# Performance work log

Hardware: AMD Instinct MI355X
Metric: run time of the kernel (lower is better)

Reference implementation:

```python
import jax, jax.numpy as jnp
import numpy as np

B, S, DIM, N, D = 1, 2688, 1536, 12, 128
C = D // 2  # 64 complex pairs per head
EPS = 1e-06


def rms_norm(x, g, eps=EPS):
    # x: [B, S, DIM] -- norm over full model dim, as in WanRMSNorm
    xf = x.astype(jnp.float32)
    return (xf * jax.lax.rsqrt(jnp.mean(xf * xf, axis=-1, keepdims=True) + eps)) * g


def rope_apply(x, f, h, w, freqs_c):
    # x: [B, S, N, D]; freqs_c: complex64 [1024, C]; f*h*w == S (full-seq case)
    s1 = C - 2 * (C // 3)  # 22 (temporal)
    s2 = C // 3            # 21 (height), 21 (width)
    ff = freqs_c[:f, :s1]
    fh = freqs_c[:h, s1:s1 + s2]
    fw = freqs_c[:w, s1 + s2:]
    fi = jnp.concatenate([
        jnp.broadcast_to(ff[:, None, None, :], (f, h, w, s1)),
        jnp.broadcast_to(fh[None, :, None, :], (f, h, w, s2)),
        jnp.broadcast_to(fw[None, None, :, :], (f, h, w, s2)),
    ], axis=-1).reshape(f * h * w, 1, C)  # [S, 1, C]
    xr = x.astype(jnp.float32).reshape(B, S, N, C, 2)
    xc = jax.lax.complex(xr[..., 0], xr[..., 1])          # [B, S, N, C]
    out = xc * fi[None]                                    # broadcast over B, N
    return jnp.stack([out.real, out.imag], axis=-1).reshape(B, S, N, D)


def setup_inputs() -> dict:
    key = jax.random.key(0)
    ks = jax.random.split(key, 12)
    w_scale = 0.02
    # deterministic rope angles (faithful structure: exp(i*theta) per axis slice)
    pos = np.arange(1024, dtype=np.float32)
    inv = 1.0 / (10000.0 ** (np.arange(C, dtype=np.float32) / C))
    ang = pos[:, None] * inv[None, :]
    return {
        "x": jax.random.normal(ks[0], (B, S, DIM), jnp.float32),
        "seq_lens": jnp.full((B,), S, dtype=jnp.int32),
        "grid_sizes": jnp.array([[6, 16, 28]], dtype=jnp.int32),
        "freqs_cos": jnp.asarray(np.cos(ang), jnp.float32),
        "freqs_sin": jnp.asarray(np.sin(ang), jnp.float32),
        "Wq": jax.random.normal(ks[1], (DIM, DIM), jnp.float32) * w_scale,
        "bq": jnp.zeros((DIM,), jnp.float32),
        "Wk": jax.random.normal(ks[2], (DIM, DIM), jnp.float32) * w_scale,
        "bk": jnp.zeros((DIM,), jnp.float32),
        "Wv": jax.random.normal(ks[3], (DIM, DIM), jnp.float32) * w_scale,
        "bv": jnp.zeros((DIM,), jnp.float32),
        "Wo": jax.random.normal(ks[4], (DIM, DIM), jnp.float32) * w_scale,
        "bo": jnp.zeros((DIM,), jnp.float32),
        "gq": jnp.ones((DIM,), jnp.float32),
        "gk": jnp.ones((DIM,), jnp.float32),
    }


def reference(x, seq_lens, grid_sizes, freqs_cos, freqs_sin,
              Wq, bq, Wk, bk, Wv, bv, Wo, bo, gq, gk):
    f, h, w = (int(grid_sizes[0, 0]), int(grid_sizes[0, 1]), int(grid_sizes[0, 2]))
    freqs_c = jax.lax.complex(freqs_cos, freqs_sin)  # [1024, C]

    q = rms_norm(x @ Wq.T + bq, gq).reshape(B, S, N, D)
    k = rms_norm(x @ Wk.T + bk, gk).reshape(B, S, N, D)
    v = (x @ Wv.T + bv).reshape(B, S, N, D)

    q = rope_apply(q, f, h, w, freqs_c)
    k = rope_apply(k, f, h, w, freqs_c)

    # SDPA with key-length masking (k_lens)
    scale = 1.0 / jnp.sqrt(jnp.float32(D))
    scores = jnp.einsum("bqnd,bknd->bnqk", q, k) * scale  # [B, N, S, S]
    kmask = jnp.arange(S)[None, :] < seq_lens[:, None]     # [B, S]
    scores = jnp.where(kmask[:, None, None, :], scores, -jnp.inf)
    attn = jax.nn.softmax(scores, axis=-1)
    out = jnp.einsum("bnqk,bknd->bqnd", attn, v).reshape(B, S, DIM)
    return out @ Wo.T + bo
```

## Files before the change

### kernel.cpp

```cpp
#include <hip/hip_runtime.h>
#include <hip/hip_bf16.h>
#include <stdint.h>

#define S_LEN 2688
#define DIM   1536
#define NH    12
#define HD    128
#define QKV_N 4608

typedef __attribute__((ext_vector_type(8)))  short bf16x8;
typedef __attribute__((ext_vector_type(4)))  float f32x4;
typedef __attribute__((ext_vector_type(16))) float f32x16;

__device__ inline ushort f2bf(float f) {
    uint32_t u = __float_as_uint(f);
    uint32_t r = (u + 0x7fffu + ((u >> 16) & 1u)) >> 16;
    return (ushort)r;
}
__device__ inline float bf2f(uint u) { return __uint_as_float(u << 16); }
__device__ inline float fexp2(float x) {
    float r;
    asm("v_exp_f32 %0, %1" : "=v"(r) : "v"(x));
    return r;
}
__device__ inline uint cvtpk(float lo, float hi) {
    uint r;
    asm("v_cvt_pk_bf16_f32 %0, %1, %2" : "=v"(r) : "v"(lo), "v"(hi));
    return r;
}

#define GLOAD16(gp, lp) __builtin_amdgcn_global_load_lds( \
    (__attribute__((address_space(1))) const void*)(gp),  \
    (__attribute__((address_space(3))) void*)(lp), 16, 0, 0)

__global__ __launch_bounds__(256) void convert_all(
    const float* __restrict__ x,
    const float* __restrict__ wq, const float* __restrict__ wk,
    const float* __restrict__ wv, const float* __restrict__ wo,
    ushort* __restrict__ xb, ushort* __restrict__ wb)
{
    const size_t NX4 = (size_t)S_LEN * DIM / 4;
    const size_t NW4 = (size_t)DIM * DIM / 4;
    size_t i = (size_t)blockIdx.x * 256 + threadIdx.x;
    const float* src; ushort* dst;
    if (i < NX4)            { src = x;  dst = xb; }
    else if (i < NX4+1*NW4) { src = wq; dst = wb;                        i -= NX4; }
    else if (i < NX4+2*NW4) { src = wk; dst = wb + 1*(size_t)DIM*DIM;    i -= NX4+1*NW4; }
    else if (i < NX4+3*NW4) { src = wv; dst = wb + 2*(size_t)DIM*DIM;    i -= NX4+2*NW4; }
    else if (i < NX4+4*NW4) { src = wo; dst = wb + 3*(size_t)DIM*DIM;    i -= NX4+3*NW4; }
    else return;
    float4 v = reinterpret_cast<const float4*>(src)[i];
    ushort4 o = { f2bf(v.x), f2bf(v.y), f2bf(v.z), f2bf(v.w) };
    reinterpret_cast<ushort4*>(dst)[i] = o;
}

__global__ __launch_bounds__(256) void gemm_qkv(
    const ushort* __restrict__ A, const ushort* __restrict__ B,
    const float* __restrict__ bq, const float* __restrict__ bk,
    const float* __restrict__ bv,
    ushort* __restrict__ qkb, ushort* __restrict__ v_t, int K)
{
    __shared__ ushort At[2][128 * 64];
    __shared__ ushort Bt[2][128 * 64];
    const int tid  = threadIdx.x;
    const int wave = tid >> 6, lane = tid & 63;
    const int lid  = blockIdx.y * 21 + blockIdx.x;
    const int xcd  = lid & 7, pos = lid >> 3;
    const int wgid = (xcd < 4 ? xcd * 95 : 4 * 95 + (xcd - 4) * 94) + pos;
    const int m0 = (wgid % 21) * 128, n0 = (wgid / 21) * 128;
    const int wr = wave >> 1, wc = wave & 1;
    const int r = lane & 15, g = lane >> 4;
    const int swz = r & 7;
    const int sj_row[4] = { (0*256+tid)>>3, (1*256+tid)>>3,
                            (2*256+tid)>>3, (3*256+tid)>>3 };
    const int sj_w = tid & 7;

    f32x4 acc[4][4] = {};
    const int NT = K >> 6;

#define STAGE_G(buf, kb)                                                      \
    do {                                                                      \
        const ushort* Ag = A + (size_t)m0 * K + (kb);                         \
        const ushort* Bg = B + (size_t)n0 * K + (kb);                         \
        _Pragma("unroll")                                                     \
        for (int t = 0; t < 4; ++t) {                                         \
            int row = sj_row[t];                                              \
            GLOAD16(Ag + (size_t)row * K + ((sj_w ^ (row & 7)) * 8),          \
                    &At[buf][(t*256 + tid) * 8]);                             \
        }                                                                     \
        _Pragma("unroll")                                                     \
        for (int t = 0; t < 4; ++t) {                                         \
            int row = sj_row[t];                                              \
            GLOAD16(Bg + (size_t)row * K + ((sj_w ^ (row & 7)) * 8),          \
                    &Bt[buf][(t*256 + tid) * 8]);                             \
        }                                                                     \
    } while (0)

    STAGE_G(0, 0);
    asm volatile("s_waitcnt vmcnt(0)" ::: "memory");
    __syncthreads();

    int cur = 0;
    for (int kt = 0; kt < NT; ++kt) {
        if (kt + 1 < NT) STAGE_G(cur ^ 1, (kt+1) * 64);
#pragma unroll
        for (int kk = 0; kk < 2; ++kk) {
            bf16x8 af[4], bfr[4];
#pragma unroll
            for (int i = 0; i < 4; ++i)
                af[i] = *reinterpret_cast<const bf16x8*>(
                    &At[cur][(wr*64 + i*16 + r) * 64 + ((kk*4 + g) ^ swz) * 8]);
#pragma unroll
            for (int i = 0; i < 4; ++i)
                bfr[i] = *reinterpret_cast<const bf16x8*>(
                    &Bt[cur][(wc*64 + i*16 + r) * 64 + ((kk*4 + g) ^ swz) * 8]);
#pragma unroll
            for (int mi = 0; mi < 4; ++mi)
#pragma unroll
                for (int ni = 0; ni < 4; ++ni)
                    acc[mi][ni] = __builtin_amdgcn_mfma_f32_16x16x32_bf16(
                        af[mi], bfr[ni], acc[mi][ni], 0, 0, 0);
        }
        if (kt + 1 < NT) {
            asm volatile("s_waitcnt vmcnt(0)" ::: "memory");
            __syncthreads();
            cur ^= 1;
        }
    }
#undef STAGE_G

    if (n0 < 2*DIM) {
#pragma unroll
        for (int ni = 0; ni < 4; ++ni) {
            int col = n0 + wc*64 + ni*16 + r;
            float bias = (col < DIM) ? bq[col] : bk[col - DIM];
#pragma unroll
            for (int mi = 0; mi < 4; ++mi) {
                int row = m0 + wr*64 + mi*16 + g*4;
#pragma unroll
                for (int j = 0; j < 4; ++j)
                    qkb[(size_t)(row + j) * (2*DIM) + col] =
                        f2bf(acc[mi][ni][j] + bias);
            }
        }
    } else {
#pragma unroll
        for (int ni = 0; ni < 4; ++ni) {
            int d = n0 - 2*DIM + wc*64 + ni*16 + r;
            float bias = bv[d];
#pragma unroll
            for (int mi = 0; mi < 4; ++mi) {
                int row = m0 + wr*64 + mi*16 + g*4;
                uint2 pkt;
                pkt.x = cvtpk(acc[mi][ni][0] + bias, acc[mi][ni][1] + bias);
                pkt.y = cvtpk(acc[mi][ni][2] + bias, acc[mi][ni][3] + bias);
                *reinterpret_cast<uint2*>(&v_t[(size_t)d * S_LEN + row]) = pkt;
            }
        }
    }
}

__global__ __launch_bounds__(256) void gemm_bt2(
    const ushort* __restrict__ A, const ushort* __restrict__ B,
    const float* __restrict__ b0,
    float* __restrict__ C, int M, int N, int K)
{
    __shared__ ushort At[128 * 64];
    __shared__ ushort Bt[64 * 64];
    const int tid  = threadIdx.x;
    const int wave = tid >> 6, lane = tid & 63;
    const int m0 = blockIdx.x * 128, n0 = blockIdx.y * 64;
    const int wr = wave >> 1, wc = wave & 1;
    const int r = lane & 15, g = lane >> 4;
    const int srow = wave * 8 + (lane >> 3);
    const int scol = (lane & 7) * 8;
    const int brow[2] = { (0*256+tid)>>3, (1*256+tid)>>3 };
    const int bcol = (tid & 7) * 8;

    f32x4 acc[4][2] = {};

    for (int k0 = 0; k0 < K; k0 += 64) {
        const ushort* Ag = A + (size_t)m0 * K + k0;
        const ushort* Bg = B + (size_t)n0 * K + k0;
#pragma unroll
        for (int t = 0; t < 4; ++t)
            GLOAD16(Ag + (size_t)(t*32 + srow) * K + scol, &At[t*2048 + wave*512]);
#pragma unroll
        for (int t = 0; t < 2; ++t)
            GLOAD16(Bg + (size_t)brow[t] * K + bcol, &Bt[(t*256 + wave*64) * 8]);
        asm volatile("s_waitcnt vmcnt(0)" ::: "memory");
        __syncthreads();
#pragma unroll
        for (int kk = 0; kk < 2; ++kk) {
            bf16x8 af[4], bfr[2];
#pragma unroll
            for (int i = 0; i < 4; ++i)
                af[i] = *reinterpret_cast<const bf16x8*>(
                    &At[(wr*64 + i*16 + r) * 64 + kk*32 + g*8]);
#pragma unroll
            for (int i = 0; i < 2; ++i)
                bfr[i] = *reinterpret_cast<const bf16x8*>(
                    &Bt[(wc*32 + i*16 + r) * 64 + kk*32 + g*8]);
#pragma unroll
            for (int mi = 0; mi < 4; ++mi)
#pragma unroll
                for (int ni = 0; ni < 2; ++ni)
                    acc[mi][ni] = __builtin_amdgcn_mfma_f32_16x16x32_bf16(
                        af[mi], bfr[ni], acc[mi][ni], 0, 0, 0);
        }
        __syncthreads();
    }

#pragma unroll
    for (int ni = 0; ni < 2; ++ni) {
        int col = n0 + wc*32 + ni*16 + r;
        float bias = b0[col];
#pragma unroll
        for (int mi = 0; mi < 4; ++mi) {
            int row = m0 + wr*64 + mi*16 + g*4;
#pragma unroll
            for (int j = 0; j < 4; ++j)
                C[(size_t)(row + j) * N + col] = acc[mi][ni][j] + bias;
        }
    }
}

__global__ __launch_bounds__(256) void normrope(
    const ushort* __restrict__ qkb, const int* __restrict__ gsz,
    const float* __restrict__ gq, const float* __restrict__ gk,
    const float* __restrict__ fcos, const float* __restrict__ fsin,
    ushort* __restrict__ q_r, ushort* __restrict__ k_r)
{
    const int s   = blockIdx.x;
    const int tid = threadIdx.x;
    const int wave = tid >> 6, lane = tid & 63;
    const uint* qrow = reinterpret_cast<const uint*>(qkb + (size_t)s * (2*DIM));
    const uint* krow = qrow + DIM/2;

    float2 qv[3], kv[3];
    float sq = 0.f, sk = 0.f;
#pragma unroll
    for (int i = 0; i < 3; ++i) {
        int p = tid + i*256;
        uint uq = qrow[p], uk = krow[p];
        qv[i].x = bf2f(uq & 0xffffu); qv[i].y = bf2f(uq >> 16);
        kv[i].x = bf2f(uk & 0xffffu); kv[i].y = bf2f(uk >> 16);
        sq += qv[i].x*qv[i].x + qv[i].y*qv[i].y;
        sk += kv[i].x*kv[i].x + kv[i].y*kv[i].y;
    }
#pragma unroll
    for (int off = 1; off < 64; off <<= 1) {
        sq += __shfl_xor(sq, off);
        sk += __shfl_xor(sk, off);
    }
    __shared__ float red[4][2];
    if (lane == 0) { red[wave][0] = sq; red[wave][1] = sk; }
    __syncthreads();
    sq = red[0][0] + red[1][0] + red[2][0] + red[3][0];
    sk = red[0][1] + red[1][1] + red[2][1] + red[3][1];
    const float rmsq = rsqrtf(sq * (1.f/DIM) + 1e-6f);
    const float rmsk = rsqrtf(sk * (1.f/DIM) + 1e-6f);

    const int hh = gsz[1], ww = gsz[2];
    const int fidx = s / (hh*ww), rem = s % (hh*ww);
    const int hidx = rem / ww,  widx = rem % ww;
    const float qscale = rmsq * (0.08838834764831845f * 1.4426950408889634f);

#pragma unroll
    for (int i = 0; i < 3; ++i) {
        int p = tid + i*256;
        int c = p & 63, head = p >> 6;
        int coord = (c < 22) ? fidx : (c < 43) ? hidx : widx;
        float cv = fcos[coord*64 + c], sv = fsin[coord*64 + c];
        float2 gqv = reinterpret_cast<const float2*>(gq)[p];
        float2 gkv = reinterpret_cast<const float2*>(gk)[p];
        float a = qv[i].x * qscale * gqv.x, b = qv[i].y * qscale * gqv.y;
        uint qo = cvtpk(a*cv - b*sv, a*sv + b*cv);
        a = kv[i].x * rmsk * gkv.x; b = kv[i].y * rmsk * gkv.y;
        uint ko = cvtpk(a*cv - b*sv, a*sv + b*cv);
        size_t off = (((size_t)head * S_LEN + s) * HD + 2*c) >> 1;
        reinterpret_cast<uint*>(q_r)[off] = qo;
        reinterpret_cast<uint*>(k_r)[off] = ko;
    }
}

__global__ __launch_bounds__(256) void attn_fwd(
    const ushort* __restrict__ q_r, const ushort* __restrict__ k_r,
    const ushort* __restrict__ v_t, const int* __restrict__ seq_lens,
    ushort* __restrict__ attn_out)
{
    __shared__ ushort Kl[2][64 * 128];
    __shared__ ushort Vl[2][128 * 64];
    const int tid  = threadIdx.x;
    const int wave = tid >> 6, lane = tid & 63;
    const int n  = blockIdx.y;
    const int seq = seq_lens[0];
    const int khalf = wave & 1, pair = wave >> 1;
    const int ql = lane & 31, h = lane >> 5, sw = lane & 7;
    const int qrow = blockIdx.x * 64 + pair * 32 + ql;
    const ushort* Qh = q_r + (size_t)n * S_LEN * HD;
    const ushort* Kh = k_r + (size_t)n * S_LEN * HD;
    const ushort* Vh = v_t + (size_t)n * HD * S_LEN;

    const int kj_row[4] = { (0*256+tid)>>4, (1*256+tid)>>4, (2*256+tid)>>4, (3*256+tid)>>4 };
    const int kj_w  = tid & 15;
    const int vj_d[4]  = { (0*256+tid)>>3, (1*256+tid)>>3, (2*256+tid)>>3, (3*256+tid)>>3 };
    const int vj_w  = tid & 7;

    bf16x8 qf[8];
#pragma unroll
    for (int c = 0; c < 8; ++c)
        qf[c] = *reinterpret_cast<const bf16x8*>(Qh + (size_t)qrow * HD + c*16 + h*8);

    f32x16 oacc[4] = {};
    float mrun = -1e30f, lrun = 0.f;

    const int nt = (seq + 63) >> 6;

#define STAGE(buf, kbase)                                                     \
    do {                                                                      \
        _Pragma("unroll")                                                     \
        for (int t = 0; t < 4; ++t) {                                         \
            int row = kj_row[t];                                              \
            GLOAD16(Kh + (size_t)((kbase) + row) * HD + ((kj_w ^ (row & 7)) * 8), \
                    &Kl[buf][(t*256 + wave*64) * 8]);                         \
        }                                                                     \
        _Pragma("unroll")                                                     \
        for (int t = 0; t < 4; ++t) {                                         \
            int d = vj_d[t];                                                  \
            GLOAD16(Vh + (size_t)d * S_LEN + (kbase) + ((vj_w ^ (d & 7)) * 8), \
                    &Vl[buf][(t*256 + wave*64) * 8]);                         \
        }                                                                     \
    } while (0)

    STAGE(0, 0);
    asm volatile("s_waitcnt vmcnt(0)" ::: "memory");
    __syncthreads();

    int cur = 0;
    for (int kt = 0; kt < nt; ++kt) {
        const int k0 = kt * 64 + khalf * 32;
        if (kt + 1 < nt) STAGE(cur ^ 1, (kt+1) * 64);

        f32x16 sf = {};
        const ushort* kl = &Kl[cur][(khalf*32 + ql) * 128];
#pragma unroll
        for (int c = 0; c < 8; ++c)
            sf = __builtin_amdgcn_mfma_f32_32x32x16_bf16(
                *reinterpret_cast<const bf16x8*>(kl + ((2*c + h) ^ sw) * 8),
                qf[c], sf, 0, 0, 0);
        if (k0 + 32 > seq) {
#pragma unroll
            for (int j = 0; j < 16; ++j)
                if (k0 + (j&3) + 8*(j>>2) + 4*h >= seq) sf[j] = -1e30f;
        }
        float pm = sf[0];
#pragma unroll
        for (int j = 1; j < 16; ++j) pm = fmaxf(pm, sf[j]);
        pm = fmaxf(pm, __shfl_xor(pm, 32));
        if (!__all(pm - mrun <= 8.f)) {
            float mn = fmaxf(mrun, pm);
            float scl = fexp2(mrun - mn);
            mrun = mn;
            lrun *= scl;
#pragma unroll
            for (int db = 0; db < 4; ++db)
#pragma unroll
                for (int j = 0; j < 16; ++j) oacc[db][j] *= scl;
        }
        float ps = 0.f;
#pragma unroll
        for (int j = 0; j < 16; ++j) {
            float e = fexp2(sf[j] - mrun);
            sf[j] = e;
            ps += e;
        }
        ps += __shfl_xor(ps, 32);
        lrun += ps;
        uint u0 = cvtpk(sf[0],  sf[1]),  u1 = cvtpk(sf[2],  sf[3]);
        uint u2 = cvtpk(sf[4],  sf[5]),  u3 = cvtpk(sf[6],  sf[7]);
        uint u4 = cvtpk(sf[8],  sf[9]),  u5 = cvtpk(sf[10], sf[11]);
        uint u6 = cvtpk(sf[12], sf[13]), u7 = cvtpk(sf[14], sf[15]);
        asm("v_permlane32_swap_b32 %0, %1" : "+v"(u0), "+v"(u2));
        asm("v_permlane32_swap_b32 %0, %1" : "+v"(u1), "+v"(u3));
        asm("v_permlane32_swap_b32 %0, %1" : "+v"(u4), "+v"(u6));
        asm("v_permlane32_swap_b32 %0, %1" : "+v"(u5), "+v"(u7));
        union { uint uu[4]; bf16x8 v; } fa, fb;
        fa.uu[0] = u0; fa.uu[1] = u1; fa.uu[2] = u2; fa.uu[3] = u3;
        fb.uu[0] = u4; fb.uu[1] = u5; fb.uu[2] = u6; fb.uu[3] = u7;
#pragma unroll
        for (int db = 0; db < 4; ++db) {
            const ushort* vl = &Vl[cur][(db*32 + ql) * 64];
            oacc[db] = __builtin_amdgcn_mfma_f32_32x32x16_bf16(
                *reinterpret_cast<const bf16x8*>(vl + ((khalf*4 + 0 + h) ^ sw) * 8),
                fa.v, oacc[db], 0, 0, 0);
            oacc[db] = __builtin_amdgcn_mfma_f32_32x32x16_bf16(
                *reinterpret_cast<const bf16x8*>(vl + ((khalf*4 + 2 + h) ^ sw) * 8),
                fb.v, oacc[db], 0, 0, 0);
        }

        if (kt + 1 < nt) {
            asm volatile("s_waitcnt vmcnt(0)" ::: "memory");
            __syncthreads();
            cur ^= 1;
        }
    }
#undef STAGE

    __syncthreads();
    float* Obuf  = (float*)&Kl[0][0];
    float* MLbuf = (float*)&Vl[0][0];
    if (khalf == 1) {
#pragma unroll
        for (int db = 0; db < 4; ++db)
#pragma unroll
            for (int j = 0; j < 16; ++j) {
                int d = db*32 + (j&3) + 8*(j>>2) + 4*h;
                Obuf[pair*4096 + d*32 + ql] = oacc[db][j];
            }
        if (h == 0) { MLbuf[pair*64 + ql] = mrun; MLbuf[pair*64 + 32 + ql] = lrun; }
    }
    __syncthreads();
    if (khalf == 0) {
        float m2 = MLbuf[pair*64 + ql], l2 = MLbuf[pair*64 + 32 + ql];
        float mm = fmaxf(mrun, m2);
        float s1 = fexp2(mrun - mm), s2 = fexp2(m2 - mm);
        float ltot = lrun * s1 + l2 * s2;
        float inv = (ltot > 0.f) ? 1.f / ltot : 0.f;
#pragma unroll
        for (int db = 0; db < 4; ++db)
#pragma unroll
            for (int j = 0; j < 16; ++j) {
                int d = db*32 + (j&3) + 8*(j>>2) + 4*h;
                oacc[db][j] = (oacc[db][j] * s1 +
                               Obuf[pair*4096 + d*32 + ql] * s2) * inv;
            }
#pragma unroll
        for (int db = 0; db < 4; ++db)
#pragma unroll
            for (int jg = 0; jg < 4; ++jg) {
                uint2 pkt;
                pkt.x = cvtpk(oacc[db][jg*4+0], oacc[db][jg*4+1]);
                pkt.y = cvtpk(oacc[db][jg*4+2], oacc[db][jg*4+3]);
                *reinterpret_cast<uint2*>(
                    &attn_out[(size_t)qrow * DIM + n*HD + db*32 + jg*8 + 4*h]) = pkt;
            }
    }
}

extern "C" void kernel_launch(void* const* d_in, const int* in_sizes, int n_in,
                              void* d_out, int out_size, void* d_ws, size_t ws_size,
                              hipStream_t stream)
{
    const float* x    = (const float*)d_in[0];
    const int*   seqL = (const int*)  d_in[1];
    const int*   gsz  = (const int*)  d_in[2];
    const float* fcos = (const float*)d_in[3];
    const float* fsin = (const float*)d_in[4];
    const float* Wq   = (const float*)d_in[5];
    const float* bq   = (const float*)d_in[6];
    const float* Wk   = (const float*)d_in[7];
    const float* bk   = (const float*)d_in[8];
    const float* Wv   = (const float*)d_in[9];
    const float* bv   = (const float*)d_in[10];
    const float* Wo   = (const float*)d_in[11];
    const float* bo   = (const float*)d_in[12];
    const float* gq   = (const float*)d_in[13];
    const float* gk   = (const float*)d_in[14];
    float* out = (float*)d_out;

    char* ws = (char*)d_ws;
    ushort* xb  = (ushort*)ws;
    ushort* wb  = xb  + (size_t)S_LEN * DIM;
    ushort* qkb = wb  + 4*(size_t)DIM*DIM;
    ushort* v_t = qkb + (size_t)S_LEN * 2*DIM;
    ushort* q_r = v_t + (size_t)DIM * S_LEN;
    ushort* k_r = q_r + (size_t)S_LEN * DIM;
    ushort* ao  = k_r + (size_t)S_LEN * DIM;

    convert_all<<<13248, 256, 0, stream>>>(x, Wq, Wk, Wv, Wo, xb, wb);
    gemm_qkv<<<dim3(21, 36), 256, 0, stream>>>(xb, wb, bq, bk, bv,
                                               qkb, v_t, DIM);
    normrope<<<S_LEN, 256, 0, stream>>>(qkb, gsz, gq, gk, fcos, fsin, q_r, k_r);
    attn_fwd<<<dim3(42, 12), 256, 0, stream>>>(q_r, k_r, v_t, seqL, ao);
    gemm_bt2<<<dim3(21, 24), 256, 0, stream>>>(ao, wb + 3*(size_t)DIM*DIM,
                                               bo, out, S_LEN, DIM, DIM);
}
```

Before: 192.9 us.

## Double-buffer LDS tiles and XOR-swizzle layout in output projection GEMM

```diff
diff --git a/kernel.cpp b/kernel.cpp
--- a/kernel.cpp
+++ b/kernel.cpp
@@ -165,42 +165,57 @@
     const float* __restrict__ b0,
     float* __restrict__ C, int M, int N, int K)
 {
-    __shared__ ushort At[128 * 64];
-    __shared__ ushort Bt[64 * 64];
+    __shared__ ushort At[2][128 * 64];
+    __shared__ ushort Bt[2][64 * 64];
     const int tid  = threadIdx.x;
     const int wave = tid >> 6, lane = tid & 63;
     const int m0 = blockIdx.x * 128, n0 = blockIdx.y * 64;
     const int wr = wave >> 1, wc = wave & 1;
     const int r = lane & 15, g = lane >> 4;
-    const int srow = wave * 8 + (lane >> 3);
-    const int scol = (lane & 7) * 8;
-    const int brow[2] = { (0*256+tid)>>3, (1*256+tid)>>3 };
-    const int bcol = (tid & 7) * 8;
+    const int swz = r & 7;
+    const int sj_row[4] = { (0*256+tid)>>3, (1*256+tid)>>3,
+                            (2*256+tid)>>3, (3*256+tid)>>3 };
+    const int sj_w = tid & 7;
 
     f32x4 acc[4][2] = {};
-
-    for (int k0 = 0; k0 < K; k0 += 64) {
-        const ushort* Ag = A + (size_t)m0 * K + k0;
-        const ushort* Bg = B + (size_t)n0 * K + k0;
-#pragma unroll
-        for (int t = 0; t < 4; ++t)
-            GLOAD16(Ag + (size_t)(t*32 + srow) * K + scol, &At[t*2048 + wave*512]);
-#pragma unroll
-        for (int t = 0; t < 2; ++t)
-            GLOAD16(Bg + (size_t)brow[t] * K + bcol, &Bt[(t*256 + wave*64) * 8]);
-        asm volatile("s_waitcnt vmcnt(0)" ::: "memory");
-        __syncthreads();
+    const int NT = K >> 6;
+
+#define STAGE_G2(buf, kb)                                                     \
+    do {                                                                      \
+        const ushort* Ag = A + (size_t)m0 * K + (kb);                         \
+        const ushort* Bg = B + (size_t)n0 * K + (kb);                         \
+        _Pragma("unroll")                                                     \
+        for (int t = 0; t < 4; ++t) {                                         \
+            int row = sj_row[t];                                              \
+            GLOAD16(Ag + (size_t)row * K + ((sj_w ^ (row & 7)) * 8),          \
+                    &At[buf][(t*256 + tid) * 8]);                             \
+        }                                                                     \
+        _Pragma("unroll")                                                     \
+        for (int t = 0; t < 2; ++t) {                                         \
+            int row = sj_row[t];                                              \
+            GLOAD16(Bg + (size_t)row * K + ((sj_w ^ (row & 7)) * 8),          \
+                    &Bt[buf][(t*256 + tid) * 8]);                             \
+        }                                                                     \
+    } while (0)
+
+    STAGE_G2(0, 0);
+    asm volatile("s_waitcnt vmcnt(0)" ::: "memory");
+    __syncthreads();
+
+    int cur = 0;
+    for (int kt = 0; kt < NT; ++kt) {
+        if (kt + 1 < NT) STAGE_G2(cur ^ 1, (kt+1) * 64);
 #pragma unroll
         for (int kk = 0; kk < 2; ++kk) {
             bf16x8 af[4], bfr[2];
 #pragma unroll
             for (int i = 0; i < 4; ++i)
                 af[i] = *reinterpret_cast<const bf16x8*>(
-                    &At[(wr*64 + i*16 + r) * 64 + kk*32 + g*8]);
+                    &At[cur][(wr*64 + i*16 + r) * 64 + ((kk*4 + g) ^ swz) * 8]);
 #pragma unroll
             for (int i = 0; i < 2; ++i)
                 bfr[i] = *reinterpret_cast<const bf16x8*>(
-                    &Bt[(wc*32 + i*16 + r) * 64 + kk*32 + g*8]);
+                    &Bt[cur][(wc*32 + i*16 + r) * 64 + ((kk*4 + g) ^ swz) * 8]);
 #pragma unroll
             for (int mi = 0; mi < 4; ++mi)
 #pragma unroll
@@ -208,8 +223,13 @@
                     acc[mi][ni] = __builtin_amdgcn_mfma_f32_16x16x32_bf16(
                         af[mi], bfr[ni], acc[mi][ni], 0, 0, 0);
         }
-        __syncthreads();
-    }
+        if (kt + 1 < NT) {
+            asm volatile("s_waitcnt vmcnt(0)" ::: "memory");
+            __syncthreads();
+            cur ^= 1;
+        }
+    }
+#undef STAGE_G2
 
 #pragma unroll
     for (int ni = 0; ni < 2; ++ni) {
```

Result: faster. 187.3 us, median of 2 (-2.9%).
